# Kernel tuning notes

Hardware: AMD Instinct MI355X
Metric: run time of the kernel (lower is better)

Reference implementation:

```python
import jax, jax.numpy as jnp
import numpy as np

DIM = 2048
NUM_HEADS = 16
HEAD_DIM = 128
MAX_SEQ_LEN = 2048
ATTN_SCALE = 0.12
EPS = 1e-6


def _rms_norm(x):
    # RMSNorm without learned weight, over last dim
    return x * jax.lax.rsqrt(jnp.mean(jnp.square(x), axis=-1, keepdims=True) + EPS)


def _rope_tables(T):
    # half of the head dim rotates, half is identity (zero frequency)
    quarter = HEAD_DIM // 4
    angular_freq = (1.0 / 1024.0) ** jnp.linspace(0.0, 1.0, quarter, dtype=jnp.float32)
    angular_freq = jnp.concatenate([angular_freq, jnp.zeros(quarter, dtype=jnp.float32)])  # [D/2]
    t = jnp.arange(T, dtype=jnp.float32)
    theta = t[:, None] * angular_freq[None, :]  # [T, D/2]
    return jnp.cos(theta), jnp.sin(theta)


def _apply_rope(x, cos, sin):
    # x: [B, T, H, D]; cos/sin: [T, D/2] -> broadcast [1, T, 1, D/2]
    x1, x2 = jnp.split(x, 2, axis=-1)
    c = cos[None, :, None, :]
    s = sin[None, :, None, :]
    y1 = x1 * c + x2 * s
    y2 = -x1 * s + x2 * c
    return jnp.concatenate([y1, y2], axis=-1)


def setup_inputs() -> dict:
    key = jax.random.key(0)
    k1, k2, k3, k4 = jax.random.split(key, 4)
    hdim = NUM_HEADS * HEAD_DIM
    x = jax.random.normal(k1, (1, MAX_SEQ_LEN, DIM), dtype=jnp.float32)
    qkvo_w = jax.random.normal(k2, (4, hdim, DIM), dtype=jnp.float32) * (DIM ** -0.5)
    ve = jax.random.normal(k3, (1, MAX_SEQ_LEN, hdim), dtype=jnp.float32)
    lambdas = jax.random.uniform(k4, (2,), dtype=jnp.float32)
    return {"x": x, "qkvo_w": qkvo_w, "ve": ve, "lambdas": lambdas}


def reference(x, qkvo_w, ve, lambdas):
    B, T, _ = x.shape
    H, D = NUM_HEADS, HEAD_DIM
    # fused qkv projection: [B, T, 3*H*D]
    qkv = jnp.einsum('btc,ehc->bteh', x, qkvo_w[:3]).reshape(B, T, 3, H, D)
    q, k, v = qkv[:, :, 0], qkv[:, :, 1], qkv[:, :, 2]  # each [B, T, H, D]
    q, k, v = _rms_norm(q), _rms_norm(k), _rms_norm(v)
    cos, sin = _rope_tables(T)
    q = _apply_rope(q, cos, sin)
    k = _apply_rope(k, cos, sin)
    v = lambdas[0] * v + lambdas[1] * ve.reshape(B, T, H, D)
    # causal attention with fixed scale
    scores = jnp.einsum('bthd,bshd->bhts', q, k) * ATTN_SCALE  # [B, H, T, T]
    causal = jnp.tril(jnp.ones((T, T), dtype=bool))
    scores = jnp.where(causal[None, None], scores, -jnp.inf)
    p = jax.nn.softmax(scores, axis=-1)
    y = jnp.einsum('bhts,bshd->bthd', p, v).reshape(B, T, H * D)
    return jnp.einsum('bth,ch->btc', y, qkvo_w[3])
```

## Files before the change

### kernel.cpp

```cpp
#include <hip/hip_runtime.h>
#include <math.h>

#define SEQ  2048
#define CDIM 2048
#define NH   16
#define DH   128
#define HDIM 2048

typedef __attribute__((ext_vector_type(8))) short  bf16x8;
typedef __attribute__((ext_vector_type(4))) float  f32x4;
typedef unsigned short ushort_t;

__device__ __forceinline__ unsigned short f2bf(float f) {
  unsigned u = __float_as_uint(f);
  u = (u + 0x7fffu + ((u >> 16) & 1u)) >> 16;
  return (unsigned short)u;
}
__device__ __forceinline__ float b2f(unsigned short s) {
  return __uint_as_float((unsigned)s << 16);
}

__device__ __forceinline__ void async_ld16(const ushort_t* g, ushort_t* l) {
  __builtin_amdgcn_global_load_lds((const __attribute__((address_space(1))) unsigned int*)g,
                                   (__attribute__((address_space(3))) unsigned int*)l,
                                   16, 0, 0);
}

__device__ __forceinline__ f32x4 mfma16(bf16x8 a, bf16x8 b, f32x4 c) {
  return __builtin_amdgcn_mfma_f32_16x16x32_bf16(a, b, c, 0, 0, 0);
}

__global__ __launch_bounds__(256) void rope_tables(float* __restrict__ cosT,
                                                   float* __restrict__ sinT) {
  int idx = blockIdx.x * 256 + threadIdx.x;
  int t = idx >> 5, d = idx & 31;
  float freq = powf(1.0f / 1024.0f, (float)d * (1.0f / 31.0f));
  float th = (float)t * freq;
  cosT[idx] = cosf(th);
  sinT[idx] = sinf(th);
}

__global__ __launch_bounds__(256) void to_bf16(const float* __restrict__ src,
                                               ushort_t* __restrict__ dst, int n8) {
  int i = blockIdx.x * 256 + threadIdx.x;
  if (i >= n8) return;
  const float4* s = (const float4*)src;
  float4 f0 = s[i * 2], f1 = s[i * 2 + 1];
  bf16x8 o;
  o[0] = (short)f2bf(f0.x); o[1] = (short)f2bf(f0.y);
  o[2] = (short)f2bf(f0.z); o[3] = (short)f2bf(f0.w);
  o[4] = (short)f2bf(f1.x); o[5] = (short)f2bf(f1.y);
  o[6] = (short)f2bf(f1.z); o[7] = (short)f2bf(f1.w);
  *(bf16x8*)&dst[i * 8] = o;
}

__global__ __launch_bounds__(256) void gemm_qkv(const ushort_t* __restrict__ A,
                                                const ushort_t* __restrict__ B,
                                                ushort_t* __restrict__ qkvb,
                                                ushort_t* __restrict__ vbT,
                                                const float* __restrict__ ve,
                                                const float* __restrict__ lambdas,
                                                const float* __restrict__ cosT,
                                                const float* __restrict__ sinT) {
  constexpr int K = CDIM;
  __shared__ __align__(16) ushort_t As[2][128 * 32];
  __shared__ __align__(16) ushort_t Bs[2][128 * 32];
  __shared__ float red[4][4][4][4];
  const int z = blockIdx.z;
  const ushort_t* Bp = B + (long)z * HDIM * CDIM;
  const int m0 = blockIdx.y * 128, n0 = blockIdx.x * 128;
  const int tid = threadIdx.x, lane = tid & 63, wave = tid >> 6;
  const int wm = wave >> 1, wn = wave & 1;
  const int g = lane >> 4, l15 = lane & 15;
  const int srow = tid >> 2, scc = tid & 3;

  auto stageG = [&](int buf, int k0) {
    int r0 = srow, r1 = srow + 64;
    int c0 = scc ^ ((r0 >> 1) & 3), c1 = scc ^ ((r1 >> 1) & 3);
    async_ld16(&A [(long)(m0 + r0) * K + k0 + c0 * 8], &As[buf][wave * 512]);
    async_ld16(&A [(long)(m0 + r1) * K + k0 + c1 * 8], &As[buf][2048 + wave * 512]);
    async_ld16(&Bp[(long)(n0 + r0) * K + k0 + c0 * 8], &Bs[buf][wave * 512]);
    async_ld16(&Bp[(long)(n0 + r1) * K + k0 + c1 * 8], &Bs[buf][2048 + wave * 512]);
  };

  f32x4 acc[4][4];
#pragma unroll
  for (int i = 0; i < 4; ++i)
#pragma unroll
    for (int j = 0; j < 4; ++j) acc[i][j] = (f32x4)0.0f;

  stageG(0, 0);
  for (int k0 = 0; k0 < K; k0 += 32) {
    const int buf = (k0 >> 5) & 1;
    __syncthreads();
    if (k0 + 32 < K) stageG(buf ^ 1, k0 + 32);

    bf16x8 af[4], bfr[4];
#pragma unroll
    for (int mi = 0; mi < 4; ++mi) {
      int row = wm * 64 + mi * 16 + l15;
      int cc = g ^ ((row >> 1) & 3);
      af[mi] = *(const bf16x8*)&As[buf][row * 32 + cc * 8];
    }
#pragma unroll
    for (int ni = 0; ni < 4; ++ni) {
      int rowm = (ni & 1) * 16 + wn * 32 + (ni >> 1) * 64 + l15;
      int cc = g ^ ((rowm >> 1) & 3);
      bfr[ni] = *(const bf16x8*)&Bs[buf][rowm * 32 + cc * 8];
    }
#pragma unroll
    for (int mi = 0; mi < 4; ++mi)
#pragma unroll
      for (int ni = 0; ni < 4; ++ni)
        acc[mi][ni] = mfma16(af[mi], bfr[ni], acc[mi][ni]);
  }

  {
    float part[4][4];
#pragma unroll
    for (int mi = 0; mi < 4; ++mi)
#pragma unroll
      for (int r = 0; r < 4; ++r) {
        float s = 0.f;
#pragma unroll
        for (int ni = 0; ni < 4; ++ni) { float v = acc[mi][ni][r]; s += v * v; }
        part[mi][r] = s;
      }
#pragma unroll
    for (int mask = 1; mask < 16; mask <<= 1)
#pragma unroll
      for (int mi = 0; mi < 4; ++mi)
#pragma unroll
        for (int r = 0; r < 4; ++r)
          part[mi][r] += __shfl_xor(part[mi][r], mask, 64);
    __syncthreads();
    if (l15 == 0)
#pragma unroll
      for (int mi = 0; mi < 4; ++mi)
#pragma unroll
        for (int r = 0; r < 4; ++r) red[wave][mi][g][r] = part[mi][r];
    __syncthreads();
  }
  float scl[4][4];
#pragma unroll
  for (int mi = 0; mi < 4; ++mi)
#pragma unroll
    for (int r = 0; r < 4; ++r)
      scl[mi][r] = rsqrtf((red[wm * 2][mi][g][r] + red[wm * 2 + 1][mi][g][r]) *
                              (1.0f / 128.0f) + 1e-6f);

  if (z < 2) {
    ushort_t* dst = qkvb + (long)z * SEQ * HDIM;
#pragma unroll
    for (int ni2 = 0; ni2 < 2; ++ni2) {
      int c = ni2 * 16 + wn * 32 + l15;
      const bool rot = (c < 32);
#pragma unroll
      for (int mi = 0; mi < 4; ++mi)
#pragma unroll
        for (int r = 0; r < 4; ++r) {
          int tt = m0 + wm * 64 + mi * 16 + g * 4 + r;
          float co = rot ? cosT[tt * 32 + c] : 1.0f;
          float si = rot ? sinT[tt * 32 + c] : 0.0f;
          float x1 = acc[mi][ni2][r] * scl[mi][r];
          float x2 = acc[mi][ni2 + 2][r] * scl[mi][r];
          dst[(long)tt * HDIM + n0 + c]      = f2bf(x1 * co + x2 * si);
          dst[(long)tt * HDIM + n0 + c + 64] = f2bf(-x1 * si + x2 * co);
        }
    }
  } else {
    float l0 = lambdas[0], l1 = lambdas[1];
    ushort_t* dst = qkvb + 2L * SEQ * HDIM;
#pragma unroll
    for (int mi = 0; mi < 4; ++mi)
#pragma unroll
      for (int ni = 0; ni < 4; ++ni) {
        int c = (ni & 1) * 16 + wn * 32 + (ni >> 1) * 64 + l15;
        int t0q = m0 + wm * 64 + mi * 16 + g * 4;
        unsigned short pk[4];
#pragma unroll
        for (int r = 0; r < 4; ++r) {
          int tt = t0q + r;
          float vv = l0 * acc[mi][ni][r] * scl[mi][r] + l1 * ve[(long)tt * HDIM + n0 + c];
          unsigned short b = f2bf(vv);
          dst[(long)tt * HDIM + n0 + c] = b;
          pk[r] = b;
        }
        *(uint2*)&vbT[(long)(n0 + c) * SEQ + t0q] =
            make_uint2((unsigned)pk[0] | ((unsigned)pk[1] << 16),
                       (unsigned)pk[2] | ((unsigned)pk[3] << 16));
      }
  }
}

__global__ __launch_bounds__(256) void flash_mfma(const ushort_t* __restrict__ qkvb,
                                                  const ushort_t* __restrict__ vbT,
                                                  ushort_t* __restrict__ yb) {
  __shared__ __align__(16) ushort_t Ks[2][64 * 128];
  __shared__ __align__(16) ushort_t Vt[2][128 * 64];
  __shared__ __align__(16) ushort_t Ps[64 * 72];
  const int xp = blockIdx.x, h = blockIdx.y;
  const int tid = threadIdx.x, lane = tid & 63, wave = tid >> 6;
  const int g = lane >> 4, l15 = lane & 15;
  const ushort_t* Kg = qkvb + (long)SEQ * HDIM + (long)h * DH;
  const ushort_t* Vg = vbT + (long)h * DH * SEQ;
  const int tA = xp, tB = 31 - xp;
  const int nA = xp + 1;

  auto stage = [&](int buf, int s0) {
#pragma unroll
    for (int i = 0; i < 4; ++i) {
      int idx = i * 256 + tid;
      int rk = idx >> 4, ck = (idx & 15) ^ (rk & 7);
      async_ld16(&Kg[(long)(s0 + rk) * HDIM + ck * 8], &Ks[buf][i * 2048 + wave * 512]);
      int rv = idx >> 3, cv = (idx & 7) ^ (rv & 7);
      async_ld16(&Vg[(long)rv * SEQ + s0 + cv * 8], &Vt[buf][i * 2048 + wave * 512]);
    }
  };

  bf16x8 qf[4];
  auto loadQ = [&](int qt) {
#pragma unroll
    for (int ks = 0; ks < 4; ++ks)
      qf[ks] = *(const bf16x8*)
          &qkvb[(long)(qt * 64 + wave * 16 + l15) * HDIM + h * DH + ks * 32 + g * 8];
  };

  f32x4 oacc[8];
  float lrow = 0.f;
#pragma unroll
  for (int dt = 0; dt < 8; ++dt) oacc[dt] = (f32x4)0.0f;

  auto writeO = [&](int qt) {
    float linv[4];
#pragma unroll
    for (int r = 0; r < 4; ++r) linv[r] = 1.0f / __shfl(lrow, g * 4 + r, 64);
#pragma unroll
    for (int dt = 0; dt < 8; ++dt) {
      int row = qt * 64 + wave * 16 + g * 4;
      int col = h * DH + dt * 16 + l15;
#pragma unroll
      for (int r = 0; r < 4; ++r)
        yb[(long)(row + r) * HDIM + col] = f2bf(oacc[dt][r] * linv[r]);
    }
  };

  loadQ(tA);
  stage(0, 0);

  for (int j = 0; j < 33; ++j) {
    __syncthreads();
    int part = (j >= nA);
    int qt = part ? tB : tA;
    int s0 = (part ? (j - nA) : j) * 64;
    if (j == nA) {
      writeO(tA);
#pragma unroll
      for (int dt = 0; dt < 8; ++dt) oacc[dt] = (f32x4)0.0f;
      lrow = 0.f;
      loadQ(tB);
    }
    if (j + 1 < 33) {
      int p2 = (j + 1 >= nA);
      int s2 = ((j + 1) - (p2 ? nA : 0)) * 64;
      stage((j + 1) & 1, s2);
    }
    const ushort_t* Kc = Ks[j & 1];
    const ushort_t* Vc = Vt[j & 1];

    f32x4 st[4];
#pragma unroll
    for (int mt = 0; mt < 4; ++mt) st[mt] = (f32x4)0.0f;
#pragma unroll
    for (int ks = 0; ks < 4; ++ks)
#pragma unroll
      for (int mt = 0; mt < 4; ++mt) {
        int row = mt * 16 + l15;
        bf16x8 a = *(const bf16x8*)&Kc[row * 128 + (((ks * 4 + g) ^ (row & 7)) * 8)];
        st[mt] = mfma16(a, qf[ks], st[mt]);
      }

    const int qg = qt * 64 + wave * 16 + l15;
    const bool diag = (s0 == qt * 64);
    float psum = 0.f;
#pragma unroll
    for (int mt = 0; mt < 4; ++mt) {
      unsigned short pb[4];
#pragma unroll
      for (int r = 0; r < 4; ++r) {
        float e = (diag && (s0 + mt * 16 + g * 4 + r > qg))
                      ? 0.0f : __expf(st[mt][r] * 0.12f);
        unsigned short b = f2bf(e);
        pb[r] = b;
        psum += b2f(b);
      }
      *(uint2*)&Ps[(wave * 16 + l15) * 72 + mt * 16 + g * 4] =
          make_uint2((unsigned)pb[0] | ((unsigned)pb[1] << 16),
                     (unsigned)pb[2] | ((unsigned)pb[3] << 16));
    }
    psum += __shfl_xor(psum, 16, 64);
    psum += __shfl_xor(psum, 32, 64);
    lrow += psum;

#pragma unroll
    for (int ks2 = 0; ks2 < 2; ++ks2) {
      bf16x8 ap = *(const bf16x8*)&Ps[(wave * 16 + l15) * 72 + ks2 * 32 + g * 8];
#pragma unroll
      for (int dt = 0; dt < 8; ++dt) {
        int row = dt * 16 + l15;
        bf16x8 bv = *(const bf16x8*)&Vc[row * 64 + (((ks2 * 4 + g) ^ (row & 7)) * 8)];
        oacc[dt] = mfma16(ap, bv, oacc[dt]);
      }
    }
  }
  writeO(tB);
}

__global__ __launch_bounds__(256) void gemm_proj(const ushort_t* __restrict__ A,
                                                 const ushort_t* __restrict__ B,
                                                 float* __restrict__ C0,
                                                 float* __restrict__ C1) {
  constexpr int KH = 1024, LDK = CDIM, N = HDIM;
  __shared__ __align__(16) ushort_t As[2][128 * 32];
  __shared__ __align__(16) ushort_t Bs[2][128 * 32];
  const int z = blockIdx.z;
  const ushort_t* Ap = A + (long)z * KH;
  const ushort_t* Bp = B + (long)z * KH;
  float* Cp = z ? C1 : C0;
  const int m0 = blockIdx.y * 128, n0 = blockIdx.x * 128;
  const int tid = threadIdx.x, lane = tid & 63, wave = tid >> 6;
  const int wm = wave >> 1, wn = wave & 1;
  const int g = lane >> 4, l15 = lane & 15;
  const int srow = tid >> 2, scc = tid & 3;

  auto stageG = [&](int buf, int k0) {
    int r0 = srow, r1 = srow + 64;
    int c0 = scc ^ ((r0 >> 1) & 3), c1 = scc ^ ((r1 >> 1) & 3);
    async_ld16(&Ap[(long)(m0 + r0) * LDK + k0 + c0 * 8], &As[buf][wave * 512]);
    async_ld16(&Ap[(long)(m0 + r1) * LDK + k0 + c1 * 8], &As[buf][2048 + wave * 512]);
    async_ld16(&Bp[(long)(n0 + r0) * LDK + k0 + c0 * 8], &Bs[buf][wave * 512]);
    async_ld16(&Bp[(long)(n0 + r1) * LDK + k0 + c1 * 8], &Bs[buf][2048 + wave * 512]);
  };

  f32x4 acc[4][4];
#pragma unroll
  for (int i = 0; i < 4; ++i)
#pragma unroll
    for (int j = 0; j < 4; ++j) acc[i][j] = (f32x4)0.0f;

  stageG(0, 0);
  for (int k0 = 0; k0 < KH; k0 += 32) {
    const int buf = (k0 >> 5) & 1;
    __syncthreads();
    if (k0 + 32 < KH) stageG(buf ^ 1, k0 + 32);

    bf16x8 af[4], bfr[4];
#pragma unroll
    for (int mi = 0; mi < 4; ++mi) {
      int row = wm * 64 + mi * 16 + l15;
      int cc = g ^ ((row >> 1) & 3);
      af[mi] = *(const bf16x8*)&As[buf][row * 32 + cc * 8];
    }
#pragma unroll
    for (int ni = 0; ni < 4; ++ni) {
      int row = wn * 64 + ni * 16 + l15;
      int cc = g ^ ((row >> 1) & 3);
      bfr[ni] = *(const bf16x8*)&Bs[buf][row * 32 + cc * 8];
    }
#pragma unroll
    for (int mi = 0; mi < 4; ++mi)
#pragma unroll
      for (int ni = 0; ni < 4; ++ni)
        acc[mi][ni] = mfma16(af[mi], bfr[ni], acc[mi][ni]);
  }

#pragma unroll
  for (int mi = 0; mi < 4; ++mi)
#pragma unroll
    for (int ni = 0; ni < 4; ++ni) {
      int row = m0 + wm * 64 + mi * 16 + g * 4;
      int col = n0 + wn * 64 + ni * 16 + l15;
#pragma unroll
      for (int r = 0; r < 4; ++r)
        Cp[(long)(row + r) * N + col] = acc[mi][ni][r];
    }
}

__global__ __launch_bounds__(256) void add_out(float* __restrict__ out,
                                               const float* __restrict__ p0, int n4) {
  int i = blockIdx.x * 256 + threadIdx.x;
  if (i >= n4) return;
  float4 a = ((const float4*)out)[i];
  float4 b = ((const float4*)p0)[i];
  a.x += b.x; a.y += b.y; a.z += b.z; a.w += b.w;
  ((float4*)out)[i] = a;
}

extern "C" void kernel_launch(void* const* d_in, const int* in_sizes, int n_in,
                              void* d_out, int out_size, void* d_ws, size_t ws_size,
                              hipStream_t stream) {
  const float* x       = (const float*)d_in[0];
  const float* w       = (const float*)d_in[1];
  const float* ve      = (const float*)d_in[2];
  const float* lambdas = (const float*)d_in[3];
  float* out = (float*)d_out;

  char* ws = (char*)d_ws;
  ushort_t* qkvb = (ushort_t*)ws;
  ushort_t* xb   = (ushort_t*)(ws + 25165824);
  ushort_t* wb   = (ushort_t*)(ws + 33554432);
  ushort_t* vbT  = (ushort_t*)(ws + 67108864);
  ushort_t* yb   = xb;
  float*    p0   = (float*)ws;

  float* cosT = out;
  float* sinT = out + SEQ * 32;

  rope_tables<<<256, 256, 0, stream>>>(cosT, sinT);
  to_bf16<<<2048, 256, 0, stream>>>(x, xb, (SEQ * CDIM) / 8);
  to_bf16<<<8192, 256, 0, stream>>>(w, wb, (4 * HDIM * CDIM) / 8);
  gemm_qkv<<<dim3(16, 16, 3), 256, 0, stream>>>(xb, wb, qkvb, vbT, ve, lambdas,
                                                cosT, sinT);
  flash_mfma<<<dim3(16, 16), 256, 0, stream>>>(qkvb, vbT, yb);
  gemm_proj<<<dim3(16, 16, 2), 256, 0, stream>>>(yb, wb + 3L * HDIM * CDIM, p0, out);
  add_out<<<4096, 256, 0, stream>>>(out, p0, (SEQ * HDIM) / 4);
}
```

Measured before the change: 370.7 us.

## Load GEMM fragments directly from global into registers, dropping LDS staging

Both the QKV and output-projection GEMMs stop staging A/B tiles through shared memory with async global-to-LDS copies and barriers. Each wave now loads its MFMA fragments straight from global memory into registers, double-buffered in registers across two k-steps. This removes LDS traffic and __syncthreads. The cost is that operands shared between waves are no longer reused through LDS, so global/L2 traffic rises roughly twofold, with 16-byte strided per-lane loads and more register pressure.

```diff
diff --git a/kernel.cpp b/kernel.cpp
--- a/kernel.cpp
+++ b/kernel.cpp
@@ -63,8 +63,6 @@
                                                 const float* __restrict__ cosT,
                                                 const float* __restrict__ sinT) {
   constexpr int K = CDIM;
-  __shared__ __align__(16) ushort_t As[2][128 * 32];
-  __shared__ __align__(16) ushort_t Bs[2][128 * 32];
   __shared__ float red[4][4][4][4];
   const int z = blockIdx.z;
   const ushort_t* Bp = B + (long)z * HDIM * CDIM;
@@ -72,15 +70,19 @@
   const int tid = threadIdx.x, lane = tid & 63, wave = tid >> 6;
   const int wm = wave >> 1, wn = wave & 1;
   const int g = lane >> 4, l15 = lane & 15;
-  const int srow = tid >> 2, scc = tid & 3;
-
-  auto stageG = [&](int buf, int k0) {
-    int r0 = srow, r1 = srow + 64;
-    int c0 = scc ^ ((r0 >> 1) & 3), c1 = scc ^ ((r1 >> 1) & 3);
-    async_ld16(&A [(long)(m0 + r0) * K + k0 + c0 * 8], &As[buf][wave * 512]);
-    async_ld16(&A [(long)(m0 + r1) * K + k0 + c1 * 8], &As[buf][2048 + wave * 512]);
-    async_ld16(&Bp[(long)(n0 + r0) * K + k0 + c0 * 8], &Bs[buf][wave * 512]);
-    async_ld16(&Bp[(long)(n0 + r1) * K + k0 + c1 * 8], &Bs[buf][2048 + wave * 512]);
+
+  const ushort_t* Ar = A  + (long)(m0 + wm * 64 + l15) * K + g * 8;
+  const ushort_t* Br = Bp + (long)(n0 + wn * 32 + l15) * K + g * 8;
+
+  auto ldA = [&](bf16x8* f, int k0) {
+#pragma unroll
+    for (int mi = 0; mi < 4; ++mi)
+      f[mi] = *(const bf16x8*)&Ar[(long)mi * 16 * K + k0];
+  };
+  auto ldB = [&](bf16x8* f, int k0) {
+#pragma unroll
+    for (int ni = 0; ni < 4; ++ni)
+      f[ni] = *(const bf16x8*)&Br[(long)((ni & 1) * 16 + (ni >> 1) * 64) * K + k0];
   };
 
   f32x4 acc[4][4];
@@ -89,30 +91,22 @@
 #pragma unroll
     for (int j = 0; j < 4; ++j) acc[i][j] = (f32x4)0.0f;
 
-  stageG(0, 0);
-  for (int k0 = 0; k0 < K; k0 += 32) {
-    const int buf = (k0 >> 5) & 1;
-    __syncthreads();
-    if (k0 + 32 < K) stageG(buf ^ 1, k0 + 32);
-
-    bf16x8 af[4], bfr[4];
-#pragma unroll
-    for (int mi = 0; mi < 4; ++mi) {
-      int row = wm * 64 + mi * 16 + l15;
-      int cc = g ^ ((row >> 1) & 3);
-      af[mi] = *(const bf16x8*)&As[buf][row * 32 + cc * 8];
-    }
-#pragma unroll
-    for (int ni = 0; ni < 4; ++ni) {
-      int rowm = (ni & 1) * 16 + wn * 32 + (ni >> 1) * 64 + l15;
-      int cc = g ^ ((rowm >> 1) & 3);
-      bfr[ni] = *(const bf16x8*)&Bs[buf][rowm * 32 + cc * 8];
-    }
+  bf16x8 a0[4], b0[4], a1[4], b1[4];
+  ldA(a0, 0);  ldB(b0, 0);
+  ldA(a1, 32); ldB(b1, 32);
+  for (int k0 = 0; k0 < K; k0 += 64) {
 #pragma unroll
     for (int mi = 0; mi < 4; ++mi)
 #pragma unroll
       for (int ni = 0; ni < 4; ++ni)
-        acc[mi][ni] = mfma16(af[mi], bfr[ni], acc[mi][ni]);
+        acc[mi][ni] = mfma16(a0[mi], b0[ni], acc[mi][ni]);
+    if (k0 + 64 < K) { ldA(a0, k0 + 64); ldB(b0, k0 + 64); }
+#pragma unroll
+    for (int mi = 0; mi < 4; ++mi)
+#pragma unroll
+      for (int ni = 0; ni < 4; ++ni)
+        acc[mi][ni] = mfma16(a1[mi], b1[ni], acc[mi][ni]);
+    if (k0 + 96 < K) { ldA(a1, k0 + 96); ldB(b1, k0 + 96); }
   }
 
   {
@@ -321,25 +315,25 @@
                                                  float* __restrict__ C0,
                                                  float* __restrict__ C1) {
   constexpr int KH = 1024, LDK = CDIM, N = HDIM;
-  __shared__ __align__(16) ushort_t As[2][128 * 32];
-  __shared__ __align__(16) ushort_t Bs[2][128 * 32];
   const int z = blockIdx.z;
-  const ushort_t* Ap = A + (long)z * KH;
-  const ushort_t* Bp = B + (long)z * KH;
   float* Cp = z ? C1 : C0;
   const int m0 = blockIdx.y * 128, n0 = blockIdx.x * 128;
   const int tid = threadIdx.x, lane = tid & 63, wave = tid >> 6;
   const int wm = wave >> 1, wn = wave & 1;
   const int g = lane >> 4, l15 = lane & 15;
-  const int srow = tid >> 2, scc = tid & 3;
-
-  auto stageG = [&](int buf, int k0) {
-    int r0 = srow, r1 = srow + 64;
-    int c0 = scc ^ ((r0 >> 1) & 3), c1 = scc ^ ((r1 >> 1) & 3);
-    async_ld16(&Ap[(long)(m0 + r0) * LDK + k0 + c0 * 8], &As[buf][wave * 512]);
-    async_ld16(&Ap[(long)(m0 + r1) * LDK + k0 + c1 * 8], &As[buf][2048 + wave * 512]);
-    async_ld16(&Bp[(long)(n0 + r0) * LDK + k0 + c0 * 8], &Bs[buf][wave * 512]);
-    async_ld16(&Bp[(long)(n0 + r1) * LDK + k0 + c1 * 8], &Bs[buf][2048 + wave * 512]);
+
+  const ushort_t* Ar = A + (long)z * KH + (long)(m0 + wm * 64 + l15) * LDK + g * 8;
+  const ushort_t* Br = B + (long)z * KH + (long)(n0 + wn * 64 + l15) * LDK + g * 8;
+
+  auto ldA = [&](bf16x8* f, int k0) {
+#pragma unroll
+    for (int mi = 0; mi < 4; ++mi)
+      f[mi] = *(const bf16x8*)&Ar[(long)mi * 16 * LDK + k0];
+  };
+  auto ldB = [&](bf16x8* f, int k0) {
+#pragma unroll
+    for (int ni = 0; ni < 4; ++ni)
+      f[ni] = *(const bf16x8*)&Br[(long)ni * 16 * LDK + k0];
   };
 
   f32x4 acc[4][4];
@@ -348,30 +342,22 @@
 #pragma unroll
     for (int j = 0; j < 4; ++j) acc[i][j] = (f32x4)0.0f;
 
-  stageG(0, 0);
-  for (int k0 = 0; k0 < KH; k0 += 32) {
-    const int buf = (k0 >> 5) & 1;
-    __syncthreads();
-    if (k0 + 32 < KH) stageG(buf ^ 1, k0 + 32);
-
-    bf16x8 af[4], bfr[4];
-#pragma unroll
-    for (int mi = 0; mi < 4; ++mi) {
-      int row = wm * 64 + mi * 16 + l15;
-      int cc = g ^ ((row >> 1) & 3);
-      af[mi] = *(const bf16x8*)&As[buf][row * 32 + cc * 8];
-    }
-#pragma unroll
-    for (int ni = 0; ni < 4; ++ni) {
-      int row = wn * 64 + ni * 16 + l15;
-      int cc = g ^ ((row >> 1) & 3);
-      bfr[ni] = *(const bf16x8*)&Bs[buf][row * 32 + cc * 8];
-    }
+  bf16x8 a0[4], b0[4], a1[4], b1[4];
+  ldA(a0, 0);  ldB(b0, 0);
+  ldA(a1, 32); ldB(b1, 32);
+  for (int k0 = 0; k0 < KH; k0 += 64) {
 #pragma unroll
     for (int mi = 0; mi < 4; ++mi)
 #pragma unroll
       for (int ni = 0; ni < 4; ++ni)
-        acc[mi][ni] = mfma16(af[mi], bfr[ni], acc[mi][ni]);
+        acc[mi][ni] = mfma16(a0[mi], b0[ni], acc[mi][ni]);
+    if (k0 + 64 < KH) { ldA(a0, k0 + 64); ldB(b0, k0 + 64); }
+#pragma unroll
+    for (int mi = 0; mi < 4; ++mi)
+#pragma unroll
+      for (int ni = 0; ni < 4; ++ni)
+        acc[mi][ni] = mfma16(a1[mi], b1[ni], acc[mi][ni]);
+    if (k0 + 96 < KH) { ldA(a1, k0 + 96); ldB(b1, k0 + 96); }
   }
 
 #pragma unroll
```

After: 465.1 us. 25.5% more time.
